# Kernel optimization log

Hardware: AMD Instinct MI355X
Metric: run time of the kernel (lower is better)

Reference implementation:

```python
import jax, jax.numpy as jnp
import numpy as np

N = 100000      # nodes
E = 3200000     # edges (avg degree 32)
D_IN = 128      # input feature dim
H = 16          # hidden_size = GCN in/out channels
M = 16          # memory_size
SLOPE = 0.01    # F.leaky_relu default negative slope


def setup_inputs() -> dict:
    key = jax.random.key(0)
    ks = jax.random.split(key, 24)
    def p(i, shape):
        return jax.random.normal(ks[i], shape, dtype=jnp.float32) * 0.05
    return {
        "x": jax.random.normal(ks[0], (N, D_IN), dtype=jnp.float32),
        "edge_index": jax.random.randint(ks[1], (2, E), 0, N),
        # preprocess Linears (torch Linear: y = x @ W.T + b)
        "W1": p(2, (256, D_IN)), "b1": p(3, (256,)),
        "W2": p(4, (H, 256)),    "b2": p(5, (H,)),
        # EvolveGNN_O layer 1: memory buffer (zeros), GRU, weight_transform, GCN bias
        "mem1": jnp.zeros((M,), jnp.float32),
        "g1_Wih": p(6, (3 * M, M)), "g1_Whh": p(7, (3 * M, M)),
        "g1_bih": p(8, (3 * M,)),   "g1_bhh": p(9, (3 * M,)),
        "wt1_W": p(10, (H * H, M)), "wt1_b": p(11, (H * H,)),
        "gcn1_b": p(12, (H,)),
        # EvolveGNN_O layer 2
        "mem2": jnp.zeros((M,), jnp.float32),
        "g2_Wih": p(13, (3 * M, M)), "g2_Whh": p(14, (3 * M, M)),
        "g2_bih": p(15, (3 * M,)),   "g2_bhh": p(16, (3 * M,)),
        "wt2_W": p(17, (H * H, M)), "wt2_b": p(18, (H * H,)),
        "gcn2_b": p(19, (H,)),
        # postprocessing Linear(hidden, 2)
        "Wout": p(20, (2, H)), "bout": p(21, (2,)),
    }


def _leaky(x):
    return jnp.where(x >= 0, x, SLOPE * x)


def _gru_step(x, Wih, Whh, bih, bhh):
    # PyTorch nn.GRU single step, h0 = 0 (default when h not provided)
    h = jnp.zeros_like(x)
    gi = Wih @ x + bih
    gh = Whh @ h + bhh
    ir, iz, inn = jnp.split(gi, 3)
    hr, hz, hn = jnp.split(gh, 3)
    r = jax.nn.sigmoid(ir + hr)
    z = jax.nn.sigmoid(iz + hz)
    n = jnp.tanh(inn + r * hn)
    return (1.0 - z) * n + z * h


def _gcn(h, row, col, W, bias):
    # PyG GCNConv: linear transform, symmetric gcn_norm (self-loops already
    # appended to row/col), gather from row, scatter-add to col, add bias.
    n = h.shape[0]
    xl = h @ W.T                                          # [N, H]
    ones = jnp.ones(row.shape[0], h.dtype)
    deg = jax.ops.segment_sum(ones, col, num_segments=n)  # in-degree incl. self-loop
    dis = jnp.where(deg > 0, jax.lax.rsqrt(deg), 0.0)
    norm = dis[row] * dis[col]                            # [E + N]
    out = jax.ops.segment_sum(xl[row] * norm[:, None], col, num_segments=n)
    return out + bias


def _evolve_gcn(h, row, col, mem, Wih, Whh, bih, bhh, wtW, wtb, gcn_b):
    new_mem = _gru_step(mem, Wih, Whh, bih, bhh)          # GRU-updated memory
    Wnew = (wtW @ new_mem + wtb).reshape(H, H)            # regenerated lin.weight [out, in]
    return _gcn(h, row, col, Wnew, gcn_b)


def reference(x, edge_index, W1, b1, W2, b2,
              mem1, g1_Wih, g1_Whh, g1_bih, g1_bhh, wt1_W, wt1_b, gcn1_b,
              mem2, g2_Wih, g2_Whh, g2_bih, g2_bhh, wt2_W, wt2_b, gcn2_b,
              Wout, bout):
    n = x.shape[0]
    loops = jnp.arange(n, dtype=edge_index.dtype)
    row = jnp.concatenate([edge_index[0], loops])         # sources (+ self-loops)
    col = jnp.concatenate([edge_index[1], loops])         # targets (+ self-loops)

    h = _leaky(x @ W1.T + b1)                             # [N, 256]
    h = _leaky(h @ W2.T + b2)                             # [N, 16]
    h = _leaky(_evolve_gcn(h, row, col, mem1, g1_Wih, g1_Whh, g1_bih, g1_bhh, wt1_W, wt1_b, gcn1_b))
    h = _leaky(_evolve_gcn(h, row, col, mem2, g2_Wih, g2_Whh, g2_bih, g2_bhh, wt2_W, wt2_b, gcn2_b))
    h = h @ Wout.T + bout                                 # [N, 2]
    return jnp.sum(h, axis=-1)                            # [N]
```

## Files before the change

### kernel.cpp

```cpp
#include <hip/hip_runtime.h>
#include <math.h>

#define SLOPE 0.01f
#define BKS   256
#define BSH2  8
#define NBKMAX 512
#define BCAP  10240

typedef short  bf16x8 __attribute__((ext_vector_type(8)));
typedef float  f32x4  __attribute__((ext_vector_type(4)));

__device__ __forceinline__ float lrelu(float v) { return v >= 0.f ? v : SLOPE * v; }

__device__ __forceinline__ unsigned short f2bf(float v) {
    unsigned u = __float_as_uint(v);
    return (unsigned short)((u + 0x7FFFu + ((u >> 16) & 1u)) >> 16);
}
__device__ __forceinline__ float bf2f(unsigned short b) {
    return __uint_as_float(((unsigned)b) << 16);
}

__global__ void prep_k(const float* __restrict__ m1, const float* __restrict__ Wih1,
                       const float* __restrict__ bih1, const float* __restrict__ bhh1,
                       const float* __restrict__ m2, const float* __restrict__ Wih2,
                       const float* __restrict__ bih2, const float* __restrict__ bhh2,
                       const float* __restrict__ wtW1, const float* __restrict__ wtb1,
                       const float* __restrict__ wtW2, const float* __restrict__ wtb2,
                       const float* __restrict__ Wout, const float* __restrict__ bout,
                       const float* __restrict__ W2,
                       float* __restrict__ Wn1, float* __restrict__ Wn2,
                       float* __restrict__ wsum, float* __restrict__ bsum,
                       unsigned short* __restrict__ W2bh, unsigned short* __restrict__ W2bl,
                       int* __restrict__ bfill, int NBK) {
    __shared__ float nm[32];
    int t = threadIdx.x;
    if (t < 32) {
        int L = t >> 4, j = t & 15;
        const float* m   = L ? m2   : m1;
        const float* Wih = L ? Wih2 : Wih1;
        const float* bih = L ? bih2 : bih1;
        const float* bhh = L ? bhh2 : bhh1;
        float gr = bih[j], gz = bih[16 + j], gn = bih[32 + j];
        for (int k = 0; k < 16; ++k) {
            float mk = m[k];
            gr += Wih[j * 16 + k] * mk;
            gz += Wih[(16 + j) * 16 + k] * mk;
            gn += Wih[(32 + j) * 16 + k] * mk;
        }
        float r = 1.f / (1.f + expf(-(gr + bhh[j])));
        float z = 1.f / (1.f + expf(-(gz + bhh[16 + j])));
        float n = tanhf(gn + r * bhh[32 + j]);
        nm[t] = (1.f - z) * n;
    }
    __syncthreads();
    float s1 = wtb1[t], s2 = wtb2[t];
    for (int k = 0; k < 16; ++k) {
        s1 += wtW1[t * 16 + k] * nm[k];
        s2 += wtW2[t * 16 + k] * nm[16 + k];
    }
    Wn1[t] = s1;
    Wn2[t] = s2;
    for (int i = t; i < 4096; i += 256) {
        float v = W2[i];
        unsigned short h = f2bf(v);
        W2bh[i] = h;
        W2bl[i] = f2bf(v - bf2f(h));
    }
    if (t < 16) wsum[t] = Wout[t] + Wout[16 + t];
    if (t == 0) bsum[0] = bout[0] + bout[1];
    for (int i = t; i < NBK; i += 256) bfill[i] = i * BCAP;
}

__global__ void wsplit_k(const float* __restrict__ W1,
                         unsigned short* __restrict__ W1h,
                         unsigned short* __restrict__ W1l) {
    int i = blockIdx.x * 256 + threadIdx.x;
    float v = W1[i];
    unsigned short h = f2bf(v);
    W1h[i] = h;
    W1l[i] = f2bf(v - bf2f(h));
}

__global__ void bscat_k(const int* __restrict__ row, const int* __restrict__ col,
                        int* __restrict__ bfill, int2* __restrict__ stage,
                        int E, int NBK) {
    __shared__ int lcnt[NBKMAX];
    __shared__ int lbase[NBKMAX];
    int t = threadIdx.x;
    for (int i = t; i < NBK; i += 256) lcnt[i] = 0;
    __syncthreads();
    int base = blockIdx.x * 4096;
    int r[16], d[16], sl[16];
#pragma unroll
    for (int i = 0; i < 16; ++i) {
        int e = base + i * 256 + t;
        if (e < E) {
            r[i]  = row[e];
            d[i]  = col[e];
            sl[i] = atomicAdd(&lcnt[d[i] >> BSH2], 1);
        } else d[i] = -1;
    }
    __syncthreads();
    for (int i = t; i < NBK; i += 256)
        lbase[i] = lcnt[i] ? atomicAdd(bfill + i, lcnt[i]) : 0;
    __syncthreads();
#pragma unroll
    for (int i = 0; i < 16; ++i) {
        if (d[i] >= 0)
            stage[lbase[d[i] >> BSH2] + sl[i]] = make_int2(r[i], d[i]);
    }
}

__global__ __launch_bounds__(512) void cscan_k(const int* __restrict__ bfill,
                                               int* __restrict__ bbase2,
                                               int* __restrict__ off,
                                               int NBK, int N, int E) {
    __shared__ int s[512];
    int t = threadIdx.x;
    int v = (t < NBK) ? (bfill[t] - t * BCAP) : 0;
    s[t] = v;
    __syncthreads();
    for (int d = 1; d < 512; d <<= 1) {
        int u = (t >= d) ? s[t - d] : 0;
        __syncthreads();
        s[t] += u;
        __syncthreads();
    }
    if (t < NBK) bbase2[t] = s[t] - v;
    if (t == 0) { bbase2[NBK] = E; off[N] = E; }
}

__global__ void bproc_k(const int2* __restrict__ stage, const int* __restrict__ bbase2,
                        int* __restrict__ off, float* __restrict__ dis,
                        int* __restrict__ srcs, int N) {
    __shared__ int lh[BKS];
    __shared__ int ssc[BKS];
    const int b  = blockIdx.x;
    const int t  = threadIdx.x;
    const int sb = b * BCAP;
    const int e0 = bbase2[b];
    const int cnt = bbase2[b + 1] - e0;
    lh[t] = 0;
    __syncthreads();
    for (int i = t; i < cnt; i += 256) {
        int2 v = stage[sb + i];
        atomicAdd(&lh[v.y & (BKS - 1)], 1);
    }
    __syncthreads();
    int c = lh[t];
    ssc[t] = c;
    __syncthreads();
    for (int d = 1; d < 256; d <<= 1) {
        int u = (t >= d) ? ssc[t - d] : 0;
        __syncthreads();
        ssc[t] += u;
        __syncthreads();
    }
    int ex = ssc[t] - c;
    {
        int node = b * BKS + t;
        if (node < N) {
            off[node] = e0 + ex;
            dis[node] = rsqrtf((float)(c + 1));
        }
    }
    __syncthreads();
    lh[t] = ex;
    __syncthreads();
    for (int i = t; i < cnt; i += 256) {
        int2 w = stage[sb + i];
        int pos = e0 + atomicAdd(&lh[w.y & (BKS - 1)], 1);
        srcs[pos] = w.x;
    }
}

__global__ __launch_bounds__(512, 6) void mlp_k(
        const float* __restrict__ x,
        const unsigned short* __restrict__ W1h,
        const unsigned short* __restrict__ W1l,
        const float* __restrict__ b1,
        const unsigned short* __restrict__ W2bh,
        const unsigned short* __restrict__ W2bl,
        const float* __restrict__ b2,
        const float* __restrict__ Wn1,
        const float* __restrict__ dis,
        unsigned short* __restrict__ xl, int N) {
    __shared__ float sbuf[11008];
    unsigned short* xh  = (unsigned short*)sbuf;
    unsigned short* xlo = xh + 8704;
    unsigned short* h1h = (unsigned short*)sbuf;
    float*          h2p = sbuf + 8448;

    const int t      = threadIdx.x;
    const int nl     = t & 63;
    const int q      = __builtin_amdgcn_readfirstlane(t >> 6);
    const int lane15 = t & 15;
    const int quad   = (t & 63) >> 4;
    const int node   = blockIdx.x * 64 + nl;
    const bool valid = node < N;

    {
        const float4* x4 = (const float4*)x;
        const size_t tb = (size_t)blockIdx.x * 2048;
        unsigned* xh32 = (unsigned*)xh;
        unsigned* xl32 = (unsigned*)xlo;
#pragma unroll
        for (int kk = 0; kk < 4; ++kk) {
            int idx  = kk * 512 + t;
            int row  = idx >> 5;
            int col4 = idx & 31;
            float4 v = make_float4(0.f, 0.f, 0.f, 0.f);
            if (blockIdx.x * 64 + row < N) v = x4[tb + idx];
            unsigned short hx = f2bf(v.x), hy = f2bf(v.y);
            unsigned short hz = f2bf(v.z), hw = f2bf(v.w);
            unsigned short lx = f2bf(v.x - bf2f(hx)), ly = f2bf(v.y - bf2f(hy));
            unsigned short lz = f2bf(v.z - bf2f(hz)), lw = f2bf(v.w - bf2f(hw));
            int base = row * 68 + col4 * 2;
            *(uint2*)(xh32 + base) =
                make_uint2((unsigned)hx | ((unsigned)hy << 16),
                           (unsigned)hz | ((unsigned)hw << 16));
            *(uint2*)(xl32 + base) =
                make_uint2((unsigned)lx | ((unsigned)ly << 16),
                           (unsigned)lz | ((unsigned)lw << 16));
        }
    }
    __syncthreads();

    f32x4 acc[4][2];
#pragma unroll
    for (int mt = 0; mt < 4; ++mt)
#pragma unroll
        for (int nt = 0; nt < 2; ++nt)
            acc[mt][nt] = (f32x4){0.f, 0.f, 0.f, 0.f};

#pragma unroll
    for (int ks = 0; ks < 4; ++ks) {
        const int koff = ks * 32 + quad * 8;
#pragma unroll
        for (int mt = 0; mt < 4; ++mt) {
            bf16x8 ah = *(const bf16x8*)(xh  + (16 * mt + lane15) * 136 + koff);
            bf16x8 al = *(const bf16x8*)(xlo + (16 * mt + lane15) * 136 + koff);
#pragma unroll
            for (int nt = 0; nt < 2; ++nt) {
                size_t wo = (size_t)(q * 32 + nt * 16 + lane15) * 128 + koff;
                bf16x8 bh = *(const bf16x8*)(W1h + wo);
                bf16x8 bl = *(const bf16x8*)(W1l + wo);
                acc[mt][nt] = __builtin_amdgcn_mfma_f32_16x16x32_bf16(ah, bh, acc[mt][nt], 0, 0, 0);
                acc[mt][nt] = __builtin_amdgcn_mfma_f32_16x16x32_bf16(ah, bl, acc[mt][nt], 0, 0, 0);
                acc[mt][nt] = __builtin_amdgcn_mfma_f32_16x16x32_bf16(al, bh, acc[mt][nt], 0, 0, 0);
            }
        }
    }
    __syncthreads();

    const int kh  = q >> 2;
    const int mt2 = q & 3;
    bf16x8 w2hf[4], w2lf[4];
#pragma unroll
    for (int ks2 = 0; ks2 < 4; ++ks2) {
        int wo = lane15 * 256 + (kh * 4 + ks2) * 32 + quad * 8;
        w2hf[ks2] = *(const bf16x8*)(W2bh + wo);
        w2lf[ks2] = *(const bf16x8*)(W2bl + wo);
    }

#pragma unroll
    for (int nt = 0; nt < 2; ++nt) {
        int hu = q * 32 + nt * 16 + lane15;
        float bb = b1[hu];
#pragma unroll
        for (int mt = 0; mt < 4; ++mt) {
            int row0 = 16 * mt + quad * 4;
#pragma unroll
            for (int r = 0; r < 4; ++r) {
                float v = lrelu(acc[mt][nt][r] + bb);
                h1h[(row0 + r) * 264 + hu] = f2bf(v);
            }
        }
    }
    __syncthreads();

    f32x4 a2 = (f32x4){0.f, 0.f, 0.f, 0.f};
#pragma unroll
    for (int ks2 = 0; ks2 < 4; ++ks2) {
        const int koff = (kh * 4 + ks2) * 32 + quad * 8;
        bf16x8 ah = *(const bf16x8*)(h1h + (16 * mt2 + lane15) * 264 + koff);
        a2 = __builtin_amdgcn_mfma_f32_16x16x32_bf16(ah, w2hf[ks2], a2, 0, 0, 0);
        a2 = __builtin_amdgcn_mfma_f32_16x16x32_bf16(ah, w2lf[ks2], a2, 0, 0, 0);
    }
    {
        float* dst = h2p + kh * 1280 + (16 * mt2 + quad * 4) * 20 + lane15;
        dst[0] = a2[0]; dst[20] = a2[1]; dst[40] = a2[2]; dst[60] = a2[3];
    }
    __syncthreads();

    {
        const f32x4* pa = (const f32x4*)(h2p + nl * 20);
        const f32x4* pb = (const f32x4*)(h2p + 1280 + nl * 20);
        f32x4 s[4];
#pragma unroll
        for (int i = 0; i < 4; ++i) s[i] = pa[i] + pb[i];
        float o0 = 0.f, o1 = 0.f;
        const float* wr0 = Wn1 + (2 * q) * 16;
        const float* wr1 = Wn1 + (2 * q + 1) * 16;
#pragma unroll
        for (int j = 0; j < 16; ++j) {
            float h = lrelu(s[j >> 2][j & 3] + b2[j]);
            o0 = fmaf(wr0[j], h, o0);
            o1 = fmaf(wr1[j], h, o1);
        }
        if (valid) {
            float d = dis[node];
            unsigned pk = (unsigned)f2bf(d * o0) | ((unsigned)f2bf(d * o1) << 16);
            *(unsigned*)(xl + (size_t)node * 16 + 2 * q) = pk;
        }
    }
}

__global__ void gather1_k(const int* __restrict__ off, const int* __restrict__ srcs,
                          const float* __restrict__ dis,
                          const unsigned short* __restrict__ xin,
                          const float* __restrict__ bias, const float* __restrict__ Wn2,
                          unsigned short* __restrict__ xout, int N) {
    __shared__ float w[256];
    {
        int j = threadIdx.x >> 4, c = threadIdx.x & 15;
        w[threadIdx.x] = Wn2[c * 16 + j];
    }
    __syncthreads();
    int t = blockIdx.x * 256 + threadIdx.x;
    int n = t >> 6;
    if (n >= N) return;
    int lane = t & 63, sub = lane >> 4, c = lane & 15;
    float acc = (sub == 0) ? bf2f(xin[(size_t)n * 16 + c]) : 0.f;
    int e  = off[n] + sub;
    int e1 = off[n + 1];
    for (; e + 12 < e1; e += 16) {
        int s0 = srcs[e], s1 = srcs[e + 4], s2 = srcs[e + 8], s3 = srcs[e + 12];
        float v0 = bf2f(xin[(size_t)s0 * 16 + c]);
        float v1 = bf2f(xin[(size_t)s1 * 16 + c]);
        float v2 = bf2f(xin[(size_t)s2 * 16 + c]);
        float v3 = bf2f(xin[(size_t)s3 * 16 + c]);
        acc += (v0 + v1) + (v2 + v3);
    }
    for (; e < e1; e += 4)
        acc += bf2f(xin[(size_t)srcs[e] * 16 + c]);
    acc += __shfl_xor(acc, 16);
    acc += __shfl_xor(acc, 32);
    float d = dis[n];
    float h = lrelu(fmaf(d, acc, bias[c]));
    float o = 0.f;
#pragma unroll
    for (int j = 0; j < 16; ++j) o = fmaf(w[j * 16 + c], __shfl(h, j, 16), o);
    if (sub == 0) xout[(size_t)n * 16 + c] = f2bf(d * o);
}

__global__ void gather2_k(const int* __restrict__ off, const int* __restrict__ srcs,
                          const float* __restrict__ dis,
                          const unsigned short* __restrict__ xin,
                          const float* __restrict__ bias, const float* __restrict__ wsum,
                          const float* __restrict__ bsum, float* __restrict__ out, int N) {
    int t = blockIdx.x * 256 + threadIdx.x;
    int n = t >> 6;
    if (n >= N) return;
    int lane = t & 63, sub = lane >> 4, c = lane & 15;
    float acc = (sub == 0) ? bf2f(xin[(size_t)n * 16 + c]) : 0.f;
    int e  = off[n] + sub;
    int e1 = off[n + 1];
    for (; e + 12 < e1; e += 16) {
        int s0 = srcs[e], s1 = srcs[e + 4], s2 = srcs[e + 8], s3 = srcs[e + 12];
        float v0 = bf2f(xin[(size_t)s0 * 16 + c]);
        float v1 = bf2f(xin[(size_t)s1 * 16 + c]);
        float v2 = bf2f(xin[(size_t)s2 * 16 + c]);
        float v3 = bf2f(xin[(size_t)s3 * 16 + c]);
        acc += (v0 + v1) + (v2 + v3);
    }
    for (; e < e1; e += 4)
        acc += bf2f(xin[(size_t)srcs[e] * 16 + c]);
    acc += __shfl_xor(acc, 16);
    acc += __shfl_xor(acc, 32);
    float v = wsum[c] * lrelu(fmaf(dis[n], acc, bias[c]));
#pragma unroll
    for (int m = 1; m < 16; m <<= 1) v += __shfl_xor(v, m);
    if (lane == 0) out[n] = v + bsum[0];
}

extern "C" void kernel_launch(void* const* d_in, const int* in_sizes, int n_in,
                              void* d_out, int out_size, void* d_ws, size_t ws_size,
                              hipStream_t stream) {
    const float* x      = (const float*)d_in[0];
    const int*   edge   = (const int*)d_in[1];
    const float* W1     = (const float*)d_in[2];
    const float* b1     = (const float*)d_in[3];
    const float* W2     = (const float*)d_in[4];
    const float* b2     = (const float*)d_in[5];
    const float* mem1   = (const float*)d_in[6];
    const float* g1_Wih = (const float*)d_in[7];
    const float* g1_bih = (const float*)d_in[9];
    const float* g1_bhh = (const float*)d_in[10];
    const float* wt1_W  = (const float*)d_in[11];
    const float* wt1_b  = (const float*)d_in[12];
    const float* gcn1_b = (const float*)d_in[13];
    const float* mem2   = (const float*)d_in[14];
    const float* g2_Wih = (const float*)d_in[15];
    const float* g2_bih = (const float*)d_in[17];
    const float* g2_bhh = (const float*)d_in[18];
    const float* wt2_W  = (const float*)d_in[19];
    const float* wt2_b  = (const float*)d_in[20];
    const float* gcn2_b = (const float*)d_in[21];
    const float* Wout   = (const float*)d_in[22];
    const float* bout   = (const float*)d_in[23];
    float* out = (float*)d_out;

    const int N = in_sizes[0] / 128;
    const int E = in_sizes[1] / 2;
    const int* row = edge;
    const int* col = edge + E;

    const int NBK = (N + BKS - 1) >> BSH2;
    const int gM  = (N + 63) / 64;
    const int gG  = (N * 64 + 255) / 256;
    const int gB  = (E + 4095) / 4096;

    float* ws    = (float*)d_ws;
    float* bufA  = ws;
    float* bufB  = bufA + (size_t)N * 16;
    float* dis   = bufB + (size_t)N * 16;
    float* sm    = dis + N;
    float* Wn1   = sm;
    float* Wn2   = sm + 256;
    float* wsum  = sm + 512;
    float* bsum  = sm + 528;
    unsigned short* W2bh = (unsigned short*)(sm + 544);
    unsigned short* W2bl = (unsigned short*)(sm + 2592);
    unsigned short* W1h = (unsigned short*)(sm + 4640);
    unsigned short* W1l = (unsigned short*)(sm + 21024);
    int*   bfill = (int*)(sm + 37408);
    int*   bbase2= bfill + NBKMAX;
    int*   off   = bbase2 + NBKMAX + 1;
    int*   srcs  = off + N + 1;
    size_t stoff = (size_t)(srcs + E - (int*)d_ws);
    stoff = (stoff + 3) & ~(size_t)3;
    int2*  stage = (int2*)((int*)d_ws + stoff);

    prep_k<<<1, 256, 0, stream>>>(mem1, g1_Wih, g1_bih, g1_bhh,
                                  mem2, g2_Wih, g2_bih, g2_bhh,
                                  wt1_W, wt1_b, wt2_W, wt2_b,
                                  Wout, bout, W2, Wn1, Wn2, wsum, bsum,
                                  W2bh, W2bl, bfill, NBK);
    wsplit_k<<<128, 256, 0, stream>>>(W1, W1h, W1l);
    bscat_k<<<gB, 256, 0, stream>>>(row, col, bfill, stage, E, NBK);
    cscan_k<<<1, 512, 0, stream>>>(bfill, bbase2, off, NBK, N, E);
    bproc_k<<<NBK, 256, 0, stream>>>(stage, bbase2, off, dis, srcs, N);
    mlp_k<<<gM, 512, 0, stream>>>(x, W1h, W1l, b1, W2bh, W2bl, b2, Wn1, dis,
                                  (unsigned short*)bufA, N);
    gather1_k<<<gG, 256, 0, stream>>>(off, srcs, dis, (unsigned short*)bufA,
                                      gcn1_b, Wn2, (unsigned short*)bufB, N);
    gather2_k<<<gG, 256, 0, stream>>>(off, srcs, dis, (unsigned short*)bufB,
                                      gcn2_b, wsum, bsum, out, N);
}
```

Before: 369.8 us.

## Assign one 16-lane group per node in gathers; hoist W1 loads in MLP

The two gather kernels switch from one 64-lane wave per node (four sub-groups splitting the edges, then a cross-group shuffle reduction) to one 16-lane group per node, so each wave handles four nodes and the edge loop is unrolled by eight. This cuts launched threads by a factor of four and removes the shuffle reduction, but each node's edge list is now walked serially by one group, which can leave lanes idle when degrees are uneven. Separately, the MLP kernel reorders its MFMA loops so the W1 fragments for each output tile are loaded once into registers before the k/m loops, and its launch-bounds occupancy hint drops from 6 to 4 to give the compiler more registers.

```diff
diff --git a/kernel.cpp b/kernel.cpp
--- a/kernel.cpp
+++ b/kernel.cpp
@@ -174,7 +174,7 @@
     }
 }
 
-__global__ __launch_bounds__(512, 6) void mlp_k(
+__global__ __launch_bounds__(512, 4) void mlp_k(
         const float* __restrict__ x,
         const unsigned short* __restrict__ W1h,
         const unsigned short* __restrict__ W1l,
@@ -234,20 +234,24 @@
             acc[mt][nt] = (f32x4){0.f, 0.f, 0.f, 0.f};
 
 #pragma unroll
-    for (int ks = 0; ks < 4; ++ks) {
-        const int koff = ks * 32 + quad * 8;
-#pragma unroll
-        for (int mt = 0; mt < 4; ++mt) {
-            bf16x8 ah = *(const bf16x8*)(xh  + (16 * mt + lane15) * 136 + koff);
-            bf16x8 al = *(const bf16x8*)(xlo + (16 * mt + lane15) * 136 + koff);
-#pragma unroll
-            for (int nt = 0; nt < 2; ++nt) {
-                size_t wo = (size_t)(q * 32 + nt * 16 + lane15) * 128 + koff;
-                bf16x8 bh = *(const bf16x8*)(W1h + wo);
-                bf16x8 bl = *(const bf16x8*)(W1l + wo);
-                acc[mt][nt] = __builtin_amdgcn_mfma_f32_16x16x32_bf16(ah, bh, acc[mt][nt], 0, 0, 0);
-                acc[mt][nt] = __builtin_amdgcn_mfma_f32_16x16x32_bf16(ah, bl, acc[mt][nt], 0, 0, 0);
-                acc[mt][nt] = __builtin_amdgcn_mfma_f32_16x16x32_bf16(al, bh, acc[mt][nt], 0, 0, 0);
+    for (int nt = 0; nt < 2; ++nt) {
+        bf16x8 bh[4], bl[4];
+#pragma unroll
+        for (int ks = 0; ks < 4; ++ks) {
+            size_t wo = (size_t)(q * 32 + nt * 16 + lane15) * 128 + ks * 32 + quad * 8;
+            bh[ks] = *(const bf16x8*)(W1h + wo);
+            bl[ks] = *(const bf16x8*)(W1l + wo);
+        }
+#pragma unroll
+        for (int ks = 0; ks < 4; ++ks) {
+            const int koff = ks * 32 + quad * 8;
+#pragma unroll
+            for (int mt = 0; mt < 4; ++mt) {
+                bf16x8 ah = *(const bf16x8*)(xh  + (16 * mt + lane15) * 136 + koff);
+                bf16x8 al = *(const bf16x8*)(xlo + (16 * mt + lane15) * 136 + koff);
+                acc[mt][nt] = __builtin_amdgcn_mfma_f32_16x16x32_bf16(ah, bh[ks], acc[mt][nt], 0, 0, 0);
+                acc[mt][nt] = __builtin_amdgcn_mfma_f32_16x16x32_bf16(ah, bl[ks], acc[mt][nt], 0, 0, 0);
+                acc[mt][nt] = __builtin_amdgcn_mfma_f32_16x16x32_bf16(al, bh[ks], acc[mt][nt], 0, 0, 0);
             }
         }
     }
@@ -327,31 +331,33 @@
         w[threadIdx.x] = Wn2[c * 16 + j];
     }
     __syncthreads();
-    int t = blockIdx.x * 256 + threadIdx.x;
-    int n = t >> 6;
-    if (n >= N) return;
-    int lane = t & 63, sub = lane >> 4, c = lane & 15;
-    float acc = (sub == 0) ? bf2f(xin[(size_t)n * 16 + c]) : 0.f;
-    int e  = off[n] + sub;
-    int e1 = off[n + 1];
-    for (; e + 12 < e1; e += 16) {
-        int s0 = srcs[e], s1 = srcs[e + 4], s2 = srcs[e + 8], s3 = srcs[e + 12];
+    int g = blockIdx.x * 16 + (threadIdx.x >> 4);
+    int c = threadIdx.x & 15;
+    if (g >= N) return;
+    float acc = bf2f(xin[(size_t)g * 16 + c]);
+    int e  = off[g];
+    int e1 = off[g + 1];
+    for (; e + 7 < e1; e += 8) {
+        int s0 = srcs[e],     s1 = srcs[e + 1], s2 = srcs[e + 2], s3 = srcs[e + 3];
+        int s4 = srcs[e + 4], s5 = srcs[e + 5], s6 = srcs[e + 6], s7 = srcs[e + 7];
         float v0 = bf2f(xin[(size_t)s0 * 16 + c]);
         float v1 = bf2f(xin[(size_t)s1 * 16 + c]);
         float v2 = bf2f(xin[(size_t)s2 * 16 + c]);
         float v3 = bf2f(xin[(size_t)s3 * 16 + c]);
-        acc += (v0 + v1) + (v2 + v3);
-    }
-    for (; e < e1; e += 4)
+        float v4 = bf2f(xin[(size_t)s4 * 16 + c]);
+        float v5 = bf2f(xin[(size_t)s5 * 16 + c]);
+        float v6 = bf2f(xin[(size_t)s6 * 16 + c]);
+        float v7 = bf2f(xin[(size_t)s7 * 16 + c]);
+        acc += ((v0 + v1) + (v2 + v3)) + ((v4 + v5) + (v6 + v7));
+    }
+    for (; e < e1; ++e)
         acc += bf2f(xin[(size_t)srcs[e] * 16 + c]);
-    acc += __shfl_xor(acc, 16);
-    acc += __shfl_xor(acc, 32);
-    float d = dis[n];
+    float d = dis[g];
     float h = lrelu(fmaf(d, acc, bias[c]));
     float o = 0.f;
 #pragma unroll
     for (int j = 0; j < 16; ++j) o = fmaf(w[j * 16 + c], __shfl(h, j, 16), o);
-    if (sub == 0) xout[(size_t)n * 16 + c] = f2bf(d * o);
+    xout[(size_t)g * 16 + c] = f2bf(d * o);
 }
 
 __global__ void gather2_k(const int* __restrict__ off, const int* __restrict__ srcs,
@@ -359,29 +365,31 @@
                           const unsigned short* __restrict__ xin,
                           const float* __restrict__ bias, const float* __restrict__ wsum,
                           const float* __restrict__ bsum, float* __restrict__ out, int N) {
-    int t = blockIdx.x * 256 + threadIdx.x;
-    int n = t >> 6;
-    if (n >= N) return;
-    int lane = t & 63, sub = lane >> 4, c = lane & 15;
-    float acc = (sub == 0) ? bf2f(xin[(size_t)n * 16 + c]) : 0.f;
-    int e  = off[n] + sub;
-    int e1 = off[n + 1];
-    for (; e + 12 < e1; e += 16) {
-        int s0 = srcs[e], s1 = srcs[e + 4], s2 = srcs[e + 8], s3 = srcs[e + 12];
+    int g = blockIdx.x * 16 + (threadIdx.x >> 4);
+    int c = threadIdx.x & 15;
+    if (g >= N) return;
+    float acc = bf2f(xin[(size_t)g * 16 + c]);
+    int e  = off[g];
+    int e1 = off[g + 1];
+    for (; e + 7 < e1; e += 8) {
+        int s0 = srcs[e],     s1 = srcs[e + 1], s2 = srcs[e + 2], s3 = srcs[e + 3];
+        int s4 = srcs[e + 4], s5 = srcs[e + 5], s6 = srcs[e + 6], s7 = srcs[e + 7];
         float v0 = bf2f(xin[(size_t)s0 * 16 + c]);
         float v1 = bf2f(xin[(size_t)s1 * 16 + c]);
         float v2 = bf2f(xin[(size_t)s2 * 16 + c]);
         float v3 = bf2f(xin[(size_t)s3 * 16 + c]);
-        acc += (v0 + v1) + (v2 + v3);
-    }
-    for (; e < e1; e += 4)
+        float v4 = bf2f(xin[(size_t)s4 * 16 + c]);
+        float v5 = bf2f(xin[(size_t)s5 * 16 + c]);
+        float v6 = bf2f(xin[(size_t)s6 * 16 + c]);
+        float v7 = bf2f(xin[(size_t)s7 * 16 + c]);
+        acc += ((v0 + v1) + (v2 + v3)) + ((v4 + v5) + (v6 + v7));
+    }
+    for (; e < e1; ++e)
         acc += bf2f(xin[(size_t)srcs[e] * 16 + c]);
-    acc += __shfl_xor(acc, 16);
-    acc += __shfl_xor(acc, 32);
-    float v = wsum[c] * lrelu(fmaf(dis[n], acc, bias[c]));
+    float v = wsum[c] * lrelu(fmaf(dis[g], acc, bias[c]));
 #pragma unroll
     for (int m = 1; m < 16; m <<= 1) v += __shfl_xor(v, m);
-    if (lane == 0) out[n] = v + bsum[0];
+    if (c == 0) out[g] = v + bsum[0];
 }
 
 extern "C" void kernel_launch(void* const* d_in, const int* in_sizes, int n_in,
@@ -418,7 +426,7 @@
 
     const int NBK = (N + BKS - 1) >> BSH2;
     const int gM  = (N + 63) / 64;
-    const int gG  = (N * 64 + 255) / 256;
+    const int gG  = (N + 15) / 16;
     const int gB  = (E + 4095) / 4096;
 
     float* ws    = (float*)d_ws;
```

New measurement: 329.6 us. 10.9% less time.
